# Kernel optimization log

Measured on AMD Instinct MI355X. Metric: run time of the kernel, lower is better.

Reference implementation:

```python
import jax, jax.numpy as jnp
import numpy as np

B, T, E, H = 2, 2048, 768, 12
D = E // H  # head_dim = 64
EPS = 1e-5


def layer_norm(x, scale, shift):
    mean = x.mean(axis=-1, keepdims=True)
    # torch .var() default is unbiased (ddof=1)
    var = x.var(axis=-1, keepdims=True, ddof=1)
    return scale * (x - mean) / jnp.sqrt(var + EPS) + shift


def gelu(x):
    c = jnp.sqrt(jnp.asarray(2.0 / jnp.pi, dtype=x.dtype))
    return 0.5 * x * (1.0 + jnp.tanh(c * (x + 0.044715 * x * x * x)))


def setup_inputs() -> dict:
    key = jax.random.key(0)
    ks = jax.random.split(key, 12)
    s = 0.02
    return {
        "x": jax.random.normal(ks[0], (B, T, E), jnp.float32),
        "wq": jax.random.normal(ks[1], (E, E), jnp.float32) * s,
        "wk": jax.random.normal(ks[2], (E, E), jnp.float32) * s,
        "wv": jax.random.normal(ks[3], (E, E), jnp.float32) * s,
        "wo": jax.random.normal(ks[4], (E, E), jnp.float32) * s,
        "bo": jnp.zeros((E,), jnp.float32),
        "ln1_scale": jnp.ones((E,), jnp.float32),
        "ln1_shift": jnp.zeros((E,), jnp.float32),
        "ln2_scale": jnp.ones((E,), jnp.float32),
        "ln2_shift": jnp.zeros((E,), jnp.float32),
        "w1": jax.random.normal(ks[5], (E, 4 * E), jnp.float32) * s,
        "b1": jnp.zeros((4 * E,), jnp.float32),
        "w2": jax.random.normal(ks[6], (4 * E, E), jnp.float32) * s,
        "b2": jnp.zeros((E,), jnp.float32),
    }


def reference(x, wq, wk, wv, wo, bo, ln1_scale, ln1_shift, ln2_scale, ln2_shift,
              w1, b1, w2, b2):
    b, t, e = x.shape
    resid = x
    h = layer_norm(x, ln1_scale, ln1_shift)
    # qkv projections (no bias), split heads -> [b, H, t, D]
    q = (h @ wq).reshape(b, t, H, D).transpose(0, 2, 1, 3)
    k = (h @ wk).reshape(b, t, H, D).transpose(0, 2, 1, 3)
    v = (h @ wv).reshape(b, t, H, D).transpose(0, 2, 1, 3)
    scores = jnp.einsum("bhqd,bhkd->bhqk", q, k) / jnp.sqrt(jnp.asarray(D, x.dtype))
    causal = jnp.tril(jnp.ones((t, t), bool))
    scores = jnp.where(causal[None, None], scores, -jnp.inf)
    attn = jax.nn.softmax(scores, axis=-1)  # dropout p=0 (eval)
    ctx = jnp.einsum("bhqk,bhkd->bhqd", attn, v)
    ctx = ctx.transpose(0, 2, 1, 3).reshape(b, t, e)
    h = ctx @ wo + bo
    x = h + resid

    resid = x
    h = layer_norm(x, ln2_scale, ln2_shift)
    h = gelu(h @ w1 + b1) @ w2 + b2
    return h + resid
```

## Files before the change

kernel.cpp:

```cpp
#include <hip/hip_runtime.h>
#include <hip/hip_bf16.h>
#include <math.h>

typedef __bf16 bf16_t;
typedef __bf16 bf16x4 __attribute__((ext_vector_type(4)));
typedef __bf16 bf16x8 __attribute__((ext_vector_type(8)));
typedef float f32x4 __attribute__((ext_vector_type(4)));

#define TB 2048
#define BB 2
#define EE 768
#define HH 12
#define MM (BB * TB)
#define E3 (3 * EE)
#define E4 (4 * EE)

template <int V> struct ICst { static constexpr int value = V; };
template <int N, int I = 0, typename F>
__device__ __forceinline__ void static_for(F&& f) {
  if constexpr (I < N) {
    f(ICst<I>{});
    static_for<N, I + 1>(f);
  }
}

__global__ __launch_bounds__(256) void k_prep(
    const float* __restrict__ wq, const float* __restrict__ wk,
    const float* __restrict__ wv, const float* __restrict__ wo,
    const float* __restrict__ w1, const float* __restrict__ w2,
    bf16_t* __restrict__ wqkvT, bf16_t* __restrict__ woT,
    bf16_t* __restrict__ w1T, bf16_t* __restrict__ w2T,
    const float* __restrict__ x, const float* __restrict__ ln1s,
    const float* __restrict__ ln1b, bf16_t* __restrict__ hbf) {
  __shared__ bf16_t tile[64][72];
  int id = blockIdx.x;
  int tid = threadIdx.x;
  if (id >= 1728) {
    int wave = tid >> 6, lane = tid & 63;
    int row = (id - 1728) * 4 + wave;
    const float* xr = x + (size_t)row * EE;
    float v[12];
    float s = 0.f, sq = 0.f;
#pragma unroll
    for (int i = 0; i < 12; i++) {
      float t = xr[lane + 64 * i];
      v[i] = t; s += t; sq += t * t;
    }
#pragma unroll
    for (int off = 1; off < 64; off <<= 1) {
      s += __shfl_xor(s, off);
      sq += __shfl_xor(sq, off);
    }
    float mean = s * (1.f / EE);
    float var = (sq - (float)EE * mean * mean) * (1.f / (EE - 1));
    float rstd = rsqrtf(var + 1e-5f);
    bf16_t* orow = hbf + (size_t)row * EE;
#pragma unroll
    for (int i = 0; i < 12; i++) {
      int e = lane + 64 * i;
      orow[e] = (bf16_t)(ln1s[e] * (v[i] - mean) * rstd + ln1b[e]);
    }
    return;
  }
  const float* src;
  bf16_t* dst;
  int K, N, kt, nt;
  float scl = 1.f;
  if (id < 576) {
    int m = id / 144, t = id - m * 144;
    kt = (t / 12) * 64; nt = (t % 12) * 64; K = 768; N = 768;
    src = (m == 0) ? wq : (m == 1) ? wk : (m == 2) ? wv : wo;
    dst = (m < 3) ? wqkvT + (size_t)m * 768 * 768 : woT;
    if (m == 0) scl = 0.125f;
  } else if (id < 1152) {
    int t = id - 576;
    kt = (t / 48) * 64; nt = (t % 48) * 64; K = 768; N = 3072;
    src = w1; dst = w1T;
  } else {
    int t = id - 1152;
    kt = (t / 12) * 64; nt = (t % 12) * 64; K = 3072; N = 768;
    src = w2; dst = w2T;
  }
  int r = tid >> 2, c = (tid & 3) * 16;
  const float* s = src + (size_t)(kt + r) * N + nt + c;
  bf16x8 t0, t1;
#pragma unroll
  for (int j = 0; j < 8; j++) {
    t0[j] = (bf16_t)(s[j] * scl);
    t1[j] = (bf16_t)(s[8 + j] * scl);
  }
  *(bf16x8*)&tile[r][c] = t0;
  *(bf16x8*)&tile[r][c + 8] = t1;
  __syncthreads();
  bf16_t* d = dst + (size_t)(nt + r) * K + kt + c;
  bf16x8 o0, o1;
#pragma unroll
  for (int j = 0; j < 8; j++) { o0[j] = tile[c + j][r]; o1[j] = tile[c + 8 + j][r]; }
  *(bf16x8*)d = o0;
  *(bf16x8*)(d + 8) = o1;
}

template <int NITER>
__global__ __launch_bounds__(256) void k_gemm128(
    const bf16_t* __restrict__ A, const bf16_t* __restrict__ Bt,
    int M, int N, int K, int epi,
    float* __restrict__ outf, bf16_t* __restrict__ outb,
    const float* __restrict__ bias, const float* __restrict__ resid,
    bf16_t* __restrict__ vtout) {
  __shared__ bf16_t As[128 * 64];
  __shared__ bf16_t Bs[128 * 64];
  int tid = threadIdx.x;
  int wave = tid >> 6, lane = tid & 63;
  int m0 = blockIdx.y * 128, n0 = blockIdx.x * 128;
  int kOff = blockIdx.z * (NITER * 64);
  int wm = (wave >> 1) * 64, wn = (wave & 1) * 64;
  int lm = lane & 15, quad = lane >> 4;

  int srow = wave * 32 + (lane >> 3);
  int scol = (((lane & 7) ^ ((lane >> 3) & 7)) * 8);
  const bf16_t* Ap[4];
  const bf16_t* Bp[4];
  bf16_t* ldsA[4];
  bf16_t* ldsB[4];
#pragma unroll
  for (int j = 0; j < 4; j++) {
    Ap[j] = A + (size_t)(m0 + srow) * K + kOff + scol + (size_t)j * 8 * K;
    Bp[j] = Bt + (size_t)(n0 + srow) * K + kOff + scol + (size_t)j * 8 * K;
    ldsA[j] = &As[(wave * 32 + j * 8) * 64];
    ldsB[j] = &Bs[(wave * 32 + j * 8) * 64];
  }

  int aOff[2][4], bOff[2][4];
#pragma unroll
  for (int c = 0; c < 2; c++) {
    int g = ((c * 4 + quad) ^ (lm & 7)) * 8;
#pragma unroll
    for (int i = 0; i < 4; i++) {
      aOff[c][i] = (wm + i * 16 + lm) * 64 + g;
      bOff[c][i] = (wn + i * 16 + lm) * 64 + g;
    }
  }

  f32x4 acc[4][4];
#pragma unroll
  for (int i = 0; i < 4; i++)
#pragma unroll
    for (int j = 0; j < 4; j++) acc[i][j] = (f32x4){0.f, 0.f, 0.f, 0.f};

  static_for<NITER>([&](auto kc) {
    constexpr int k = decltype(kc)::value;
    __syncthreads();
#pragma unroll
    for (int j = 0; j < 4; j++) {
      __builtin_amdgcn_global_load_lds(
          (const __attribute__((address_space(1))) void*)(Ap[j] + k * 64),
          (__attribute__((address_space(3))) void*)ldsA[j], 16, 0, 0);
      __builtin_amdgcn_global_load_lds(
          (const __attribute__((address_space(1))) void*)(Bp[j] + k * 64),
          (__attribute__((address_space(3))) void*)ldsB[j], 16, 0, 0);
    }
    __syncthreads();
#pragma unroll
    for (int c = 0; c < 2; c++) {
      bf16x8 af[4], bfr[4];
#pragma unroll
      for (int i = 0; i < 4; i++) {
        af[i] = *(const bf16x8*)&As[aOff[c][i]];
        bfr[i] = *(const bf16x8*)&Bs[bOff[c][i]];
      }
#pragma unroll
      for (int i = 0; i < 4; i++)
#pragma unroll
        for (int j = 0; j < 4; j++)
          acc[i][j] = __builtin_amdgcn_mfma_f32_16x16x32_bf16(af[i], bfr[j], acc[i][j], 0, 0, 0);
    }
  });

  size_t pbase = (size_t)blockIdx.z * M * N;
  bool vtile = (epi == 0) && (n0 >= 2 * EE);
#pragma unroll
  for (int i = 0; i < 4; i++) {
#pragma unroll
    for (int j = 0; j < 4; j++) {
      int col = n0 + wn + j * 16 + lm;
      if (vtile) {
        int hv = (col - 2 * EE) >> 6, d = (col - 2 * EE) & 63;
        int row0 = m0 + wm + i * 16 + quad * 4;
        int bb = row0 >> 11, t0 = row0 & (TB - 1);
        bf16x4 v4;
#pragma unroll
        for (int r = 0; r < 4; r++) v4[r] = (bf16_t)acc[i][j][r];
        *(bf16x4*)&vtout[((size_t)(bb * HH + hv) * 64 + d) * TB + t0] = v4;
        continue;
      }
#pragma unroll
      for (int r = 0; r < 4; r++) {
        int row = m0 + wm + i * 16 + quad * 4 + r;
        size_t o = (size_t)row * N + col;
        float c = acc[i][j][r];
        if (epi == 0) {
          outb[o] = (bf16_t)c;
        } else if (epi == 1) {
          float xg = c + bias[col];
          float u2 = xg * 1.5957691216057308f + xg * xg * xg * 0.07135481627561393f;
          float t = 1.f - 2.f / (__expf(u2) + 1.f);
          outb[o] = (bf16_t)(0.5f * xg * (1.f + t));
        } else if (epi == 2) {
          outf[o] = c + bias[col] + resid[o];
        } else {
          outb[pbase + o] = (bf16_t)c;
        }
      }
    }
  }
}

__global__ __launch_bounds__(256) void k_reduce_ln2(
    const bf16_t* __restrict__ p, const float* __restrict__ bo_,
    const float* __restrict__ x, const float* __restrict__ sc,
    const float* __restrict__ sh, float* __restrict__ x1,
    bf16_t* __restrict__ h2) {
  int wave = threadIdx.x >> 6, lane = threadIdx.x & 63;
  int row = blockIdx.x * 4 + wave;
  const bf16_t* p0 = p + (size_t)row * EE;
  const bf16_t* p1 = p0 + (size_t)MM * EE;
  const float* xr = x + (size_t)row * EE;
  float v[12];
  float s = 0.f, sq = 0.f;
#pragma unroll
  for (int i = 0; i < 12; i++) {
    int e = lane + 64 * i;
    float t = (float)p0[e] + (float)p1[e] + bo_[e] + xr[e];
    v[i] = t; s += t; sq += t * t;
  }
#pragma unroll
  for (int off = 1; off < 64; off <<= 1) {
    s += __shfl_xor(s, off);
    sq += __shfl_xor(sq, off);
  }
  float mean = s * (1.f / EE);
  float var = (sq - (float)EE * mean * mean) * (1.f / (EE - 1));
  float rstd = rsqrtf(var + 1e-5f);
  float* x1r = x1 + (size_t)row * EE;
  bf16_t* h2r = h2 + (size_t)row * EE;
#pragma unroll
  for (int i = 0; i < 12; i++) {
    int e = lane + 64 * i;
    x1r[e] = v[i];
    h2r[e] = (bf16_t)(sc[e] * (v[i] - mean) * rstd + sh[e]);
  }
}

__global__ __launch_bounds__(256) void k_reduce_out(
    const bf16_t* __restrict__ p, const float* __restrict__ b2,
    const float* __restrict__ x1, float* __restrict__ out) {
  size_t e = ((size_t)blockIdx.x * 256 + threadIdx.x) * 8;
  bf16x8 a0 = *(const bf16x8*)(p + e);
  bf16x8 a1 = *(const bf16x8*)(p + (size_t)MM * EE + e);
  bf16x8 a2 = *(const bf16x8*)(p + (size_t)2 * MM * EE + e);
  bf16x8 a3 = *(const bf16x8*)(p + (size_t)3 * MM * EE + e);
  int col = (int)(e % EE);
#pragma unroll
  for (int j = 0; j < 8; j++) {
    out[e + j] = (float)a0[j] + (float)a1[j] + (float)a2[j] + (float)a3[j] +
                 b2[col + j] + x1[e + j];
  }
}

__global__ __launch_bounds__(256) void k_attn_mfma(const bf16_t* __restrict__ qkv,
                                                   const bf16_t* __restrict__ vt,
                                                   bf16_t* __restrict__ opart,
                                                   float* __restrict__ lpart) {
  __shared__ bf16_t Qs[64][72];
  __shared__ bf16_t Ks[64][72];
  __shared__ bf16_t Vt[64][72];
  __shared__ bf16_t Ps[4][16][72];

  int bh = blockIdx.x;
  int y = blockIdx.y;
  int qt, c, nsplit;
  if (y < 32)      { qt = 24 + (y >> 2); c = y & 3; nsplit = 4; }
  else if (y < 56) { int z = y - 32; qt = 16 + z / 3; c = z - (z / 3) * 3; nsplit = 3; }
  else if (y < 72) { int z = y - 56; qt = 8 + (z >> 1); c = z & 1; nsplit = 2; }
  else             { qt = y - 72; c = 0; nsplit = 1; }
  int ntiles = qt + 1;
  int len = (ntiles + nsplit - 1) / nsplit;
  int k0t = c * len;
  int k1t = k0t + len < ntiles ? k0t + len : ntiles;

  int b = bh / HH, h = bh - b * HH;
  int q0 = qt * 64;
  int tid = threadIdx.x;
  int wave = tid >> 6, lane = tid & 63;
  int lm = lane & 15, quad = lane >> 4;
  int sr = tid >> 2, sc = (tid & 3) * 16;
  const bf16_t* vt_bh = vt + (size_t)bh * 64 * TB;

  {
    const bf16_t* src = qkv + (size_t)(b * TB + q0 + sr) * E3 + h * 64 + sc;
    *(bf16x8*)(&Qs[sr][sc]) = *(const bf16x8*)src;
    *(bf16x8*)(&Qs[sr][sc + 8]) = *(const bf16x8*)(src + 8);
  }
  __syncthreads();
  bf16x8 qf0 = *(const bf16x8*)(&Qs[wave * 16 + lm][quad * 8]);
  bf16x8 qf1 = *(const bf16x8*)(&Qs[wave * 16 + lm][32 + quad * 8]);

  f32x4 o_acc[4];
#pragma unroll
  for (int nt = 0; nt < 4; nt++) o_acc[nt] = (f32x4){0.f, 0.f, 0.f, 0.f};
  float l = 0.f;

  for (int kt = k0t; kt < k1t; kt++) {
    __syncthreads();
    {
      const bf16_t* ksrc = qkv + (size_t)(b * TB + kt * 64 + sr) * E3 + EE + h * 64 + sc;
      *(bf16x8*)(&Ks[sr][sc]) = *(const bf16x8*)ksrc;
      *(bf16x8*)(&Ks[sr][sc + 8]) = *(const bf16x8*)(ksrc + 8);
      const bf16_t* vsrc = vt_bh + (size_t)sr * TB + kt * 64 + sc;
      *(bf16x8*)(&Vt[sr][sc]) = *(const bf16x8*)vsrc;
      *(bf16x8*)(&Vt[sr][sc + 8]) = *(const bf16x8*)(vsrc + 8);
    }
    __syncthreads();

    f32x4 st[4];
#pragma unroll
    for (int nt = 0; nt < 4; nt++) {
      st[nt] = (f32x4){0.f, 0.f, 0.f, 0.f};
      bf16x8 kf0 = *(const bf16x8*)(&Ks[nt * 16 + lm][quad * 8]);
      bf16x8 kf1 = *(const bf16x8*)(&Ks[nt * 16 + lm][32 + quad * 8]);
      st[nt] = __builtin_amdgcn_mfma_f32_16x16x32_bf16(kf0, qf0, st[nt], 0, 0, 0);
      st[nt] = __builtin_amdgcn_mfma_f32_16x16x32_bf16(kf1, qf1, st[nt], 0, 0, 0);
    }
    if (kt == qt) {
#pragma unroll
      for (int nt = 0; nt < 4; nt++)
#pragma unroll
        for (int r = 0; r < 4; r++)
          if (nt * 16 + quad * 4 + r > wave * 16 + lm) st[nt][r] = -1e30f;
    }

#pragma unroll
    for (int nt = 0; nt < 4; nt++) {
      bf16x4 pk;
#pragma unroll
      for (int r = 0; r < 4; r++) {
        float p = __expf(st[nt][r]);
        pk[r] = (bf16_t)p;
        l += p;
      }
      *(bf16x4*)(&Ps[wave][lm][nt * 16 + quad * 4]) = pk;
    }

    bf16x8 pf0 = *(const bf16x8*)(&Ps[wave][lm][quad * 8]);
    bf16x8 pf1 = *(const bf16x8*)(&Ps[wave][lm][32 + quad * 8]);
#pragma unroll
    for (int nt = 0; nt < 4; nt++) {
      bf16x8 vf0 = *(const bf16x8*)(&Vt[nt * 16 + lm][quad * 8]);
      bf16x8 vf1 = *(const bf16x8*)(&Vt[nt * 16 + lm][32 + quad * 8]);
      o_acc[nt] = __builtin_amdgcn_mfma_f32_16x16x32_bf16(pf0, vf0, o_acc[nt], 0, 0, 0);
      o_acc[nt] = __builtin_amdgcn_mfma_f32_16x16x32_bf16(pf1, vf1, o_acc[nt], 0, 0, 0);
    }
  }

  l += __shfl_xor(l, 16);
  l += __shfl_xor(l, 32);
  size_t slot = (size_t)(bh * 32 + qt) * 4 + c;
  if (quad == 0) lpart[slot * 64 + wave * 16 + lm] = l;
  bf16_t* ob = opart + slot * 4096;
#pragma unroll
  for (int nt = 0; nt < 4; nt++)
#pragma unroll
    for (int r = 0; r < 4; r++)
      ob[(wave * 16 + quad * 4 + r) * 64 + nt * 16 + lm] = (bf16_t)o_acc[nt][r];
}

__global__ __launch_bounds__(256) void k_attn_reduce(
    const bf16_t* __restrict__ opart, const float* __restrict__ lpart,
    bf16_t* __restrict__ ctx) {
  int bh = blockIdx.x, qt = blockIdx.y;
  int b = bh / HH, h = bh - b * HH;
  int nsplit = qt >= 24 ? 4 : qt >= 16 ? 3 : qt >= 8 ? 2 : 1;
  int tid = threadIdx.x;
  int q = tid >> 2, dc = (tid & 3) * 16;
  size_t slot0 = (size_t)(bh * 32 + qt) * 4;
  float o[16];
#pragma unroll
  for (int j = 0; j < 16; j++) o[j] = 0.f;
  float lsum = 0.f;
  for (int c = 0; c < nsplit; c++) {
    const bf16_t* p = opart + (slot0 + c) * 4096 + q * 64 + dc;
    bf16x8 u0 = *(const bf16x8*)p;
    bf16x8 u1 = *(const bf16x8*)(p + 8);
#pragma unroll
    for (int j = 0; j < 8; j++) { o[j] += (float)u0[j]; o[8 + j] += (float)u1[j]; }
    lsum += lpart[(slot0 + c) * 64 + q];
  }
  float inv = 1.f / lsum;
  bf16_t* dst = ctx + (size_t)(b * TB + qt * 64 + q) * EE + h * 64 + dc;
  bf16x8 d0, d1;
#pragma unroll
  for (int j = 0; j < 8; j++) { d0[j] = (bf16_t)(o[j] * inv); d1[j] = (bf16_t)(o[8 + j] * inv); }
  *(bf16x8*)dst = d0;
  *(bf16x8*)(dst + 8) = d1;
}

extern "C" void kernel_launch(void* const* d_in, const int* in_sizes, int n_in,
                              void* d_out, int out_size, void* d_ws, size_t ws_size,
                              hipStream_t stream) {
  const float* x    = (const float*)d_in[0];
  const float* wq   = (const float*)d_in[1];
  const float* wk   = (const float*)d_in[2];
  const float* wv   = (const float*)d_in[3];
  const float* wo   = (const float*)d_in[4];
  const float* bo   = (const float*)d_in[5];
  const float* ln1s = (const float*)d_in[6];
  const float* ln1b = (const float*)d_in[7];
  const float* ln2s = (const float*)d_in[8];
  const float* ln2b = (const float*)d_in[9];
  const float* w1   = (const float*)d_in[10];
  const float* b1   = (const float*)d_in[11];
  const float* w2   = (const float*)d_in[12];
  const float* b2   = (const float*)d_in[13];
  float* out = (float*)d_out;

  char* ws = (char*)d_ws;
  size_t off = 0;
  auto alloc = [&](size_t bytes) {
    char* p = ws + off;
    off += (bytes + 255) & ~(size_t)255;
    return p;
  };
  float*  x1    = (float*) alloc((size_t)MM * EE * 4);
  bf16_t* w1T   = (bf16_t*)alloc((size_t)E4 * EE * 2);
  bf16_t* w2T   = (bf16_t*)alloc((size_t)EE * E4 * 2);
  bf16_t* woT   = (bf16_t*)alloc((size_t)EE * EE * 2);
  bf16_t* wqkvT = (bf16_t*)alloc((size_t)E3 * EE * 2);
  bf16_t* hbf   = (bf16_t*)alloc((size_t)MM * EE * 2);
  bf16_t* h2    = (bf16_t*)alloc((size_t)MM * EE * 2);
  bf16_t* vtb   = (bf16_t*)alloc((size_t)BB * HH * 64 * TB * 2);
  bf16_t* part  = (bf16_t*)alloc((size_t)4 * MM * EE * 2);
  bf16_t* opart = (bf16_t*)alloc((size_t)BB * HH * 32 * 4 * 4096 * 2);
  float*  lpart = (float*) alloc((size_t)BB * HH * 32 * 4 * 64 * 4);
  bf16_t* qkv   = (bf16_t*)alloc((size_t)MM * E3 * 2);
  bf16_t* hmid  = qkv;

  k_prep<<<2752, 256, 0, stream>>>(wq, wk, wv, wo, w1, w2,
                                   wqkvT, woT, w1T, w2T, x, ln1s, ln1b, hbf);
  k_gemm128<12><<<dim3(E3 / 128, MM / 128), 256, 0, stream>>>(
      hbf, wqkvT, MM, E3, EE, 0, nullptr, qkv, nullptr, nullptr, vtb);
  k_attn_mfma<<<dim3(BB * HH, 80), 256, 0, stream>>>(qkv, vtb, opart, lpart);
  k_attn_reduce<<<dim3(BB * HH, TB / 64), 256, 0, stream>>>(opart, lpart, hbf);
  k_gemm128<6><<<dim3(EE / 128, MM / 128, 2), 256, 0, stream>>>(
      hbf, woT, MM, EE, EE, 3, nullptr, part, nullptr, nullptr, nullptr);
  k_reduce_ln2<<<MM / 4, 256, 0, stream>>>(part, bo, x, ln2s, ln2b, x1, h2);
  k_gemm128<12><<<dim3(E4 / 128, MM / 128), 256, 0, stream>>>(
      h2, w1T, MM, E4, EE, 1, nullptr, hmid, b1, nullptr, nullptr);
  k_gemm128<12><<<dim3(EE / 128, MM / 128, 4), 256, 0, stream>>>(
      hmid, w2T, MM, EE, E4, 3, nullptr, part, nullptr, nullptr, nullptr);
  k_reduce_out<<<(MM * EE / 8 + 255) / 256, 256, 0, stream>>>(part, b2, x1, out);
}
```

Measured before the change: 278.0 us.

## Replace split-K partial buffers and reduce kernels with fp32 atomic accumulation

The split-K GEMMs for the output projection and the second MLP layer now atomically add fp32 results into pre-initialized destination buffers instead of writing bf16 partials. The initial values come from earlier kernels: x1 is seeded with x + bo in the LN1 prep kernel, and out is seeded with x1 + b2 in the LN2 kernel. This removes the k_reduce_out kernel and the partial buffer traffic, at the cost of global float atomics, which contend and make the summation order nondeterministic.

```diff
diff --git a/kernel.cpp b/kernel.cpp
--- a/kernel.cpp
+++ b/kernel.cpp
@@ -31,7 +31,8 @@
     bf16_t* __restrict__ wqkvT, bf16_t* __restrict__ woT,
     bf16_t* __restrict__ w1T, bf16_t* __restrict__ w2T,
     const float* __restrict__ x, const float* __restrict__ ln1s,
-    const float* __restrict__ ln1b, bf16_t* __restrict__ hbf) {
+    const float* __restrict__ ln1b, bf16_t* __restrict__ hbf,
+    const float* __restrict__ bo_, float* __restrict__ x1) {
   __shared__ bf16_t tile[64][72];
   int id = blockIdx.x;
   int tid = threadIdx.x;
@@ -55,10 +56,12 @@
     float var = (sq - (float)EE * mean * mean) * (1.f / (EE - 1));
     float rstd = rsqrtf(var + 1e-5f);
     bf16_t* orow = hbf + (size_t)row * EE;
+    float* x1r = x1 + (size_t)row * EE;
 #pragma unroll
     for (int i = 0; i < 12; i++) {
       int e = lane + 64 * i;
       orow[e] = (bf16_t)(ln1s[e] * (v[i] - mean) * rstd + ln1b[e]);
+      x1r[e] = v[i] + bo_[e];
     }
     return;
   }
@@ -176,7 +179,6 @@
     }
   });
 
-  size_t pbase = (size_t)blockIdx.z * M * N;
   bool vtile = (epi == 0) && (n0 >= 2 * EE);
 #pragma unroll
   for (int i = 0; i < 4; i++) {
@@ -208,29 +210,25 @@
         } else if (epi == 2) {
           outf[o] = c + bias[col] + resid[o];
         } else {
-          outb[pbase + o] = (bf16_t)c;
+          atomicAdd(&outf[o], c);
         }
       }
     }
   }
 }
 
-__global__ __launch_bounds__(256) void k_reduce_ln2(
-    const bf16_t* __restrict__ p, const float* __restrict__ bo_,
-    const float* __restrict__ x, const float* __restrict__ sc,
-    const float* __restrict__ sh, float* __restrict__ x1,
-    bf16_t* __restrict__ h2) {
+__global__ __launch_bounds__(256) void k_ln2(
+    const float* __restrict__ x1, const float* __restrict__ sc,
+    const float* __restrict__ sh, const float* __restrict__ b2,
+    bf16_t* __restrict__ h2, float* __restrict__ outinit) {
   int wave = threadIdx.x >> 6, lane = threadIdx.x & 63;
   int row = blockIdx.x * 4 + wave;
-  const bf16_t* p0 = p + (size_t)row * EE;
-  const bf16_t* p1 = p0 + (size_t)MM * EE;
-  const float* xr = x + (size_t)row * EE;
+  const float* xr = x1 + (size_t)row * EE;
   float v[12];
   float s = 0.f, sq = 0.f;
 #pragma unroll
   for (int i = 0; i < 12; i++) {
-    int e = lane + 64 * i;
-    float t = (float)p0[e] + (float)p1[e] + bo_[e] + xr[e];
+    float t = xr[lane + 64 * i];
     v[i] = t; s += t; sq += t * t;
   }
 #pragma unroll
@@ -241,29 +239,13 @@
   float mean = s * (1.f / EE);
   float var = (sq - (float)EE * mean * mean) * (1.f / (EE - 1));
   float rstd = rsqrtf(var + 1e-5f);
-  float* x1r = x1 + (size_t)row * EE;
   bf16_t* h2r = h2 + (size_t)row * EE;
+  float* oir = outinit + (size_t)row * EE;
 #pragma unroll
   for (int i = 0; i < 12; i++) {
     int e = lane + 64 * i;
-    x1r[e] = v[i];
     h2r[e] = (bf16_t)(sc[e] * (v[i] - mean) * rstd + sh[e]);
-  }
-}
-
-__global__ __launch_bounds__(256) void k_reduce_out(
-    const bf16_t* __restrict__ p, const float* __restrict__ b2,
-    const float* __restrict__ x1, float* __restrict__ out) {
-  size_t e = ((size_t)blockIdx.x * 256 + threadIdx.x) * 8;
-  bf16x8 a0 = *(const bf16x8*)(p + e);
-  bf16x8 a1 = *(const bf16x8*)(p + (size_t)MM * EE + e);
-  bf16x8 a2 = *(const bf16x8*)(p + (size_t)2 * MM * EE + e);
-  bf16x8 a3 = *(const bf16x8*)(p + (size_t)3 * MM * EE + e);
-  int col = (int)(e % EE);
-#pragma unroll
-  for (int j = 0; j < 8; j++) {
-    out[e + j] = (float)a0[j] + (float)a1[j] + (float)a2[j] + (float)a3[j] +
-                 b2[col + j] + x1[e + j];
+    oir[e] = v[i] + b2[e];
   }
 }
 
@@ -438,24 +420,23 @@
   bf16_t* hbf   = (bf16_t*)alloc((size_t)MM * EE * 2);
   bf16_t* h2    = (bf16_t*)alloc((size_t)MM * EE * 2);
   bf16_t* vtb   = (bf16_t*)alloc((size_t)BB * HH * 64 * TB * 2);
-  bf16_t* part  = (bf16_t*)alloc((size_t)4 * MM * EE * 2);
   bf16_t* opart = (bf16_t*)alloc((size_t)BB * HH * 32 * 4 * 4096 * 2);
   float*  lpart = (float*) alloc((size_t)BB * HH * 32 * 4 * 64 * 4);
   bf16_t* qkv   = (bf16_t*)alloc((size_t)MM * E3 * 2);
   bf16_t* hmid  = qkv;
 
   k_prep<<<2752, 256, 0, stream>>>(wq, wk, wv, wo, w1, w2,
-                                   wqkvT, woT, w1T, w2T, x, ln1s, ln1b, hbf);
+                                   wqkvT, woT, w1T, w2T, x, ln1s, ln1b, hbf,
+                                   bo, x1);
   k_gemm128<12><<<dim3(E3 / 128, MM / 128), 256, 0, stream>>>(
       hbf, wqkvT, MM, E3, EE, 0, nullptr, qkv, nullptr, nullptr, vtb);
   k_attn_mfma<<<dim3(BB * HH, 80), 256, 0, stream>>>(qkv, vtb, opart, lpart);
   k_attn_reduce<<<dim3(BB * HH, TB / 64), 256, 0, stream>>>(opart, lpart, hbf);
   k_gemm128<6><<<dim3(EE / 128, MM / 128, 2), 256, 0, stream>>>(
-      hbf, woT, MM, EE, EE, 3, nullptr, part, nullptr, nullptr, nullptr);
-  k_reduce_ln2<<<MM / 4, 256, 0, stream>>>(part, bo, x, ln2s, ln2b, x1, h2);
+      hbf, woT, MM, EE, EE, 3, x1, nullptr, nullptr, nullptr, nullptr);
+  k_ln2<<<MM / 4, 256, 0, stream>>>(x1, ln2s, ln2b, b2, h2, out);
   k_gemm128<12><<<dim3(E4 / 128, MM / 128), 256, 0, stream>>>(
       h2, w1T, MM, E4, EE, 1, nullptr, hmid, b1, nullptr, nullptr);
   k_gemm128<12><<<dim3(EE / 128, MM / 128, 4), 256, 0, stream>>>(
-      hmid, w2T, MM, EE, E4, 3, nullptr, part, nullptr, nullptr, nullptr);
-  k_reduce_out<<<(MM * EE / 8 + 255) / 256, 256, 0, stream>>>(part, b2, x1, out);
-}
+      hmid, w2T, MM, EE, E4, 3, out, nullptr, nullptr, nullptr, nullptr);
+}
```

Measured after the change: 304.7 us. +9.6%, slower.

## Fuse split-K and attention split reductions into producers via atomic last-block counters

Applied to the files above, without the earlier changes.

Removes the separate attention-reduce and output-reduce kernels. Each split block now bumps an atomic counter, and the last one to finish sums the partials and writes the final result: normalized ctx for attention, and bias plus residual output for the FFN down-projection. Unsplit attention tiles write ctx directly. This saves two launches and some traffic, at the cost of threadfences, atomics, and a serialized reduction tail on the last-arriving block.

```diff
diff --git a/kernel.cpp b/kernel.cpp
--- a/kernel.cpp
+++ b/kernel.cpp
@@ -31,10 +31,15 @@
     bf16_t* __restrict__ wqkvT, bf16_t* __restrict__ woT,
     bf16_t* __restrict__ w1T, bf16_t* __restrict__ w2T,
     const float* __restrict__ x, const float* __restrict__ ln1s,
-    const float* __restrict__ ln1b, bf16_t* __restrict__ hbf) {
+    const float* __restrict__ ln1b, bf16_t* __restrict__ hbf,
+    int* __restrict__ cnt) {
   __shared__ bf16_t tile[64][72];
   int id = blockIdx.x;
   int tid = threadIdx.x;
+  if (id == 2752) {
+    for (int i = tid; i < 1024; i += 256) cnt[i] = 0;
+    return;
+  }
   if (id >= 1728) {
     int wave = tid >> 6, lane = tid & 63;
     int row = (id - 1728) * 4 + wave;
@@ -106,7 +111,7 @@
     int M, int N, int K, int epi,
     float* __restrict__ outf, bf16_t* __restrict__ outb,
     const float* __restrict__ bias, const float* __restrict__ resid,
-    bf16_t* __restrict__ vtout) {
+    bf16_t* __restrict__ vtout, int* __restrict__ cnt) {
   __shared__ bf16_t As[128 * 64];
   __shared__ bf16_t Bs[128 * 64];
   int tid = threadIdx.x;
@@ -213,6 +218,34 @@
       }
     }
   }
+
+  if (epi == 4) {
+    __threadfence();
+    __syncthreads();
+    __shared__ int lastFlag;
+    if (tid == 0)
+      lastFlag = (atomicAdd(&cnt[768 + blockIdx.y * gridDim.x + blockIdx.x], 1) == 3);
+    __syncthreads();
+    if (lastFlag) {
+      __threadfence();
+      int r = tid >> 1;
+      int cb = (tid & 1) * 64;
+      int colb = n0 + cb;
+      size_t rowoff = (size_t)(m0 + r) * N + colb;
+#pragma unroll
+      for (int ch = 0; ch < 8; ch++) {
+        size_t o = rowoff + ch * 8;
+        bf16x8 p0 = *(const bf16x8*)&outb[o];
+        bf16x8 p1 = *(const bf16x8*)&outb[(size_t)M * N + o];
+        bf16x8 p2 = *(const bf16x8*)&outb[(size_t)2 * M * N + o];
+        bf16x8 p3 = *(const bf16x8*)&outb[(size_t)3 * M * N + o];
+#pragma unroll
+        for (int e = 0; e < 8; e++)
+          outf[o + e] = (float)p0[e] + (float)p1[e] + (float)p2[e] + (float)p3[e] +
+                        bias[colb + ch * 8 + e] + resid[o + e];
+      }
+    }
+  }
 }
 
 __global__ __launch_bounds__(256) void k_reduce_ln2(
@@ -251,26 +284,12 @@
   }
 }
 
-__global__ __launch_bounds__(256) void k_reduce_out(
-    const bf16_t* __restrict__ p, const float* __restrict__ b2,
-    const float* __restrict__ x1, float* __restrict__ out) {
-  size_t e = ((size_t)blockIdx.x * 256 + threadIdx.x) * 8;
-  bf16x8 a0 = *(const bf16x8*)(p + e);
-  bf16x8 a1 = *(const bf16x8*)(p + (size_t)MM * EE + e);
-  bf16x8 a2 = *(const bf16x8*)(p + (size_t)2 * MM * EE + e);
-  bf16x8 a3 = *(const bf16x8*)(p + (size_t)3 * MM * EE + e);
-  int col = (int)(e % EE);
-#pragma unroll
-  for (int j = 0; j < 8; j++) {
-    out[e + j] = (float)a0[j] + (float)a1[j] + (float)a2[j] + (float)a3[j] +
-                 b2[col + j] + x1[e + j];
-  }
-}
-
 __global__ __launch_bounds__(256) void k_attn_mfma(const bf16_t* __restrict__ qkv,
                                                    const bf16_t* __restrict__ vt,
                                                    bf16_t* __restrict__ opart,
-                                                   float* __restrict__ lpart) {
+                                                   float* __restrict__ lpart,
+                                                   bf16_t* __restrict__ ctx,
+                                                   int* __restrict__ cnt) {
   __shared__ bf16_t Qs[64][72];
   __shared__ bf16_t Ks[64][72];
   __shared__ bf16_t Vt[64][72];
@@ -364,6 +383,23 @@
 
   l += __shfl_xor(l, 16);
   l += __shfl_xor(l, 32);
+
+  if (nsplit == 1) {
+    float inv = 1.f / l;
+    float inv_c[4];
+#pragma unroll
+    for (int r = 0; r < 4; r++) inv_c[r] = __shfl(inv, quad * 4 + r);
+#pragma unroll
+    for (int nt = 0; nt < 4; nt++)
+#pragma unroll
+      for (int r = 0; r < 4; r++) {
+        int row = q0 + wave * 16 + quad * 4 + r;
+        ctx[(size_t)(b * TB + row) * EE + h * 64 + nt * 16 + lm] =
+            (bf16_t)(o_acc[nt][r] * inv_c[r]);
+      }
+    return;
+  }
+
   size_t slot = (size_t)(bh * 32 + qt) * 4 + c;
   if (quad == 0) lpart[slot * 64 + wave * 16 + lm] = l;
   bf16_t* ob = opart + slot * 4096;
@@ -372,36 +408,40 @@
 #pragma unroll
     for (int r = 0; r < 4; r++)
       ob[(wave * 16 + quad * 4 + r) * 64 + nt * 16 + lm] = (bf16_t)o_acc[nt][r];
-}
-
-__global__ __launch_bounds__(256) void k_attn_reduce(
-    const bf16_t* __restrict__ opart, const float* __restrict__ lpart,
-    bf16_t* __restrict__ ctx) {
-  int bh = blockIdx.x, qt = blockIdx.y;
-  int b = bh / HH, h = bh - b * HH;
-  int nsplit = qt >= 24 ? 4 : qt >= 16 ? 3 : qt >= 8 ? 2 : 1;
-  int tid = threadIdx.x;
-  int q = tid >> 2, dc = (tid & 3) * 16;
-  size_t slot0 = (size_t)(bh * 32 + qt) * 4;
-  float o[16];
-#pragma unroll
-  for (int j = 0; j < 16; j++) o[j] = 0.f;
-  float lsum = 0.f;
-  for (int c = 0; c < nsplit; c++) {
-    const bf16_t* p = opart + (slot0 + c) * 4096 + q * 64 + dc;
-    bf16x8 u0 = *(const bf16x8*)p;
-    bf16x8 u1 = *(const bf16x8*)(p + 8);
-#pragma unroll
-    for (int j = 0; j < 8; j++) { o[j] += (float)u0[j]; o[8 + j] += (float)u1[j]; }
-    lsum += lpart[(slot0 + c) * 64 + q];
-  }
-  float inv = 1.f / lsum;
-  bf16_t* dst = ctx + (size_t)(b * TB + qt * 64 + q) * EE + h * 64 + dc;
-  bf16x8 d0, d1;
-#pragma unroll
-  for (int j = 0; j < 8; j++) { d0[j] = (bf16_t)(o[j] * inv); d1[j] = (bf16_t)(o[8 + j] * inv); }
-  *(bf16x8*)dst = d0;
-  *(bf16x8*)(dst + 8) = d1;
+
+  __threadfence();
+  __syncthreads();
+  __shared__ int lastFlag;
+  if (tid == 0)
+    lastFlag = (atomicAdd(&cnt[bh * 32 + qt], 1) == nsplit - 1);
+  __syncthreads();
+  if (lastFlag) {
+    __threadfence();
+    int q = tid >> 2, dc = (tid & 3) * 16;
+    size_t slot0 = (size_t)(bh * 32 + qt) * 4;
+    float o[16];
+#pragma unroll
+    for (int j = 0; j < 16; j++) o[j] = 0.f;
+    float lsum = 0.f;
+    for (int cc = 0; cc < nsplit; cc++) {
+      const bf16_t* p = opart + (slot0 + cc) * 4096 + q * 64 + dc;
+      bf16x8 u0 = *(const bf16x8*)p;
+      bf16x8 u1 = *(const bf16x8*)(p + 8);
+#pragma unroll
+      for (int j = 0; j < 8; j++) { o[j] += (float)u0[j]; o[8 + j] += (float)u1[j]; }
+      lsum += lpart[(slot0 + cc) * 64 + q];
+    }
+    float inv = 1.f / lsum;
+    bf16_t* dst = ctx + (size_t)(b * TB + qt * 64 + q) * EE + h * 64 + dc;
+    bf16x8 d0, d1;
+#pragma unroll
+    for (int j = 0; j < 8; j++) {
+      d0[j] = (bf16_t)(o[j] * inv);
+      d1[j] = (bf16_t)(o[8 + j] * inv);
+    }
+    *(bf16x8*)dst = d0;
+    *(bf16x8*)(dst + 8) = d1;
+  }
 }
 
 extern "C" void kernel_launch(void* const* d_in, const int* in_sizes, int n_in,
@@ -441,21 +481,20 @@
   bf16_t* part  = (bf16_t*)alloc((size_t)4 * MM * EE * 2);
   bf16_t* opart = (bf16_t*)alloc((size_t)BB * HH * 32 * 4 * 4096 * 2);
   float*  lpart = (float*) alloc((size_t)BB * HH * 32 * 4 * 64 * 4);
+  int*    cnt   = (int*)   alloc(1024 * 4);
   bf16_t* qkv   = (bf16_t*)alloc((size_t)MM * E3 * 2);
   bf16_t* hmid  = qkv;
 
-  k_prep<<<2752, 256, 0, stream>>>(wq, wk, wv, wo, w1, w2,
-                                   wqkvT, woT, w1T, w2T, x, ln1s, ln1b, hbf);
+  k_prep<<<2753, 256, 0, stream>>>(wq, wk, wv, wo, w1, w2,
+                                   wqkvT, woT, w1T, w2T, x, ln1s, ln1b, hbf, cnt);
   k_gemm128<12><<<dim3(E3 / 128, MM / 128), 256, 0, stream>>>(
-      hbf, wqkvT, MM, E3, EE, 0, nullptr, qkv, nullptr, nullptr, vtb);
-  k_attn_mfma<<<dim3(BB * HH, 80), 256, 0, stream>>>(qkv, vtb, opart, lpart);
-  k_attn_reduce<<<dim3(BB * HH, TB / 64), 256, 0, stream>>>(opart, lpart, hbf);
+      hbf, wqkvT, MM, E3, EE, 0, nullptr, qkv, nullptr, nullptr, vtb, nullptr);
+  k_attn_mfma<<<dim3(BB * HH, 80), 256, 0, stream>>>(qkv, vtb, opart, lpart, hbf, cnt);
   k_gemm128<6><<<dim3(EE / 128, MM / 128, 2), 256, 0, stream>>>(
-      hbf, woT, MM, EE, EE, 3, nullptr, part, nullptr, nullptr, nullptr);
+      hbf, woT, MM, EE, EE, 3, nullptr, part, nullptr, nullptr, nullptr, nullptr);
   k_reduce_ln2<<<MM / 4, 256, 0, stream>>>(part, bo, x, ln2s, ln2b, x1, h2);
   k_gemm128<12><<<dim3(E4 / 128, MM / 128), 256, 0, stream>>>(
-      h2, w1T, MM, E4, EE, 1, nullptr, hmid, b1, nullptr, nullptr);
+      h2, w1T, MM, E4, EE, 1, nullptr, hmid, b1, nullptr, nullptr, nullptr);
   k_gemm128<12><<<dim3(EE / 128, MM / 128, 4), 256, 0, stream>>>(
-      hmid, w2T, MM, EE, E4, 3, nullptr, part, nullptr, nullptr, nullptr);
-  k_reduce_out<<<(MM * EE / 8 + 255) / 256, 256, 0, stream>>>(part, b2, x1, out);
+      hmid, w2T, MM, EE, E4, 4, out, part, b2, x1, nullptr, cnt);
 }
```

After: 713.0 us. +156.5%, slower.
